# Kernel tuning notes

Measured on AMD Instinct MI355X. Metric: run time of the kernel, lower is better.

## Reference

```python
import jax, jax.numpy as jnp
import numpy as np

B, N, E, NREG, DIN, F = 16, 20000, 640000, 2000, 128, 32
NEG_SLOPE = 0.2  # PyG GATConv default negative_slope


def setup_inputs() -> dict:
    key = jax.random.key(0)
    ks = jax.random.split(key, 10)
    x = jax.random.normal(ks[0], (B, N, DIN), dtype=jnp.float32)
    edge_src = jnp.sort(jax.random.randint(ks[1], (E,), 0, NREG, dtype=jnp.int64))
    edge_dst = jax.random.randint(ks[2], (E,), 0, N, dtype=jnp.int64)
    edge_attr = jax.random.uniform(ks[3], (B, E, 1), dtype=jnp.float32)
    # GATConv parameters (heads=1, concat=False, edge_dim=1)
    W = jax.random.normal(ks[4], (DIN, F), dtype=jnp.float32) * 0.05   # lin (shared src/dst)
    att_src = jax.random.normal(ks[5], (F,), dtype=jnp.float32) * 0.1
    att_dst = jax.random.normal(ks[6], (F,), dtype=jnp.float32) * 0.1
    lin_edge = jax.random.normal(ks[7], (1, F), dtype=jnp.float32) * 0.1
    att_edge = jax.random.normal(ks[8], (F,), dtype=jnp.float32) * 0.1
    bias = jax.random.normal(ks[9], (F,), dtype=jnp.float32) * 0.01
    return {"x": x, "edge_attr": edge_attr, "W": W, "att_src": att_src,
            "att_dst": att_dst, "lin_edge": lin_edge, "att_edge": att_edge,
            "bias": bias, "edge_src": edge_src, "edge_dst": edge_dst}


def _gat_regulon(x, eattr, W, att_src, att_dst, lin_edge, att_edge, bias,
                 src, dst):
    # x: [N, DIN], eattr: [E, 1]; src/dst: [E] int (src < NREG, sorted)
    h = x @ W                                  # [N, F]
    a_src = h @ att_src                        # [N]
    a_dst = h @ att_dst                        # [N]
    # add_self_loops=True with fill_value='mean' for edge_attr
    loop_attr = jnp.broadcast_to(jnp.mean(eattr, axis=0, keepdims=True), (N, 1))
    eattr_full = jnp.concatenate([eattr, loop_attr], axis=0)         # [E+N, 1]
    sl = jnp.arange(N, dtype=src.dtype)
    src_f = jnp.concatenate([src, sl])                               # [E+N]
    dst_f = jnp.concatenate([dst, sl])                               # [E+N]
    a_edge = (eattr_full @ lin_edge) @ att_edge                      # [E+N]
    alpha = jax.nn.leaky_relu(a_src[src_f] + a_dst[dst_f] + a_edge, NEG_SLOPE)
    # segment softmax over destination nodes (self-loops => no empty segment)
    m = jax.ops.segment_max(alpha, dst_f, num_segments=N)
    ex = jnp.exp(alpha - m[dst_f])
    s = jax.ops.segment_sum(ex, dst_f, num_segments=N)
    coef = ex / s[dst_f]                                             # [E+N]
    rep = jax.ops.segment_sum(coef[:, None] * h[src_f], dst_f, num_segments=N)
    rep = rep + bias                                                 # [N, F]
    # fused regulon pooling: out[i] = rep[i] + sum_{(i->t) in E} rep[t]
    pooled = jax.ops.segment_sum(rep[dst], src, num_segments=NREG)   # [NREG, F]
    return rep[:NREG] + pooled


def reference(x, edge_attr, W, att_src, att_dst, lin_edge, att_edge, bias,
              edge_src, edge_dst):
    fn = jax.vmap(lambda xi, ei: _gat_regulon(xi, ei, W, att_src, att_dst,
                                              lin_edge, att_edge, bias,
                                              edge_src, edge_dst))
    return fn(x, edge_attr)                                          # [B, NREG, F]
```

## Files before the change

### kernel.cpp

```cpp
#include <hip/hip_runtime.h>
#include <hip/hip_fp16.h>
#include <math.h>

#define B    16
#define N    20000
#define E    640000
#define NREG 2000
#define DIN  128
#define F    32
#define NEG  0.2f
#define BF   (B * F)
#define NCHUNK 8
#define CS   2500
#define HIST_BLOCKS 1024
#define SCAT_BLOCKS 1024

typedef unsigned int uint;

__device__ inline uint f16pair(float a, float b) {
    __half2 h = __floats2half2_rn(a, b);
    return *(uint*)&h;
}
__device__ inline float2 h2f2(uint v) {
    return __half22float2(*(__half2*)&v);
}

__global__ __launch_bounds__(256) void k_prep1(const int* __restrict__ esrc,
                                               const int* __restrict__ edst,
                                               const float* __restrict__ eattr,
                                               const float* __restrict__ lin_edge,
                                               const float* __restrict__ att_edge,
                                               int* __restrict__ counts,
                                               int* __restrict__ roff,
                                               float* __restrict__ meanb,
                                               float* __restrict__ cedge) {
    int blk = blockIdx.x;
    int t = threadIdx.x;
    if (blk < HIST_BLOCKS) {
        {
            int b = blk >> 6, sl = blk & 63;
            const float4* base = (const float4*)(eattr + (size_t)b * E + sl * 10000);
            float s = 0.f;
            for (int i = t; i < 2500; i += 256) {
                float4 v = base[i];
                s += (v.x + v.y) + (v.z + v.w);
            }
            __shared__ float sh[256];
            sh[t] = s;
            __syncthreads();
            for (int d = 128; d > 0; d >>= 1) {
                if (t < d) sh[t] += sh[t + d];
                __syncthreads();
            }
            if (t == 0) atomicAdd(&meanb[b], sh[0]);
        }
        for (int e = blk * 256 + t; e < E; e += HIST_BLOCKS * 256)
            atomicAdd(&counts[edst[e]], 1);
    } else if (blk < HIST_BLOCKS + 8) {
        int r = (blk - HIST_BLOCKS) * 256 + t;
        if (r > NREG) return;
        int lo = 0, hi = E;
        while (lo < hi) {
            int mid = (lo + hi) >> 1;
            if (esrc[mid] < r) lo = mid + 1; else hi = mid;
        }
        roff[r] = lo;
    } else {
        if (t == 0) {
            float s = 0.f;
            for (int f = 0; f < F; ++f) s += lin_edge[f] * att_edge[f];
            *cedge = s;
        }
    }
}

__global__ __launch_bounds__(1024) void k_scan(const int* __restrict__ in,
                                               int* __restrict__ out, int n) {
    __shared__ int sh[1024];
    int t = threadIdx.x;
    int chunk = (n + 1023) / 1024;
    int lo = t * chunk;
    int hi = lo + chunk; if (hi > n) hi = n;
    int local = 0;
    for (int i = lo; i < hi; ++i) local += in[i];
    sh[t] = local;
    __syncthreads();
    for (int d = 1; d < 1024; d <<= 1) {
        int v = (t >= d) ? sh[t - d] : 0;
        __syncthreads();
        sh[t] += v;
        __syncthreads();
    }
    int run = (t == 0) ? 0 : sh[t - 1];
    for (int i = lo; i < hi; ++i) { out[i] = run; run += in[i]; }
    if (t == 1023) out[n] = sh[1023];
}

__global__ __launch_bounds__(256) void k_prep2(const int* __restrict__ esrc,
                                               const int* __restrict__ edst,
                                               const int* __restrict__ off,
                                               int* __restrict__ cursor,
                                               int2* __restrict__ csr_se,
                                               const int* __restrict__ roff,
                                               int* __restrict__ boff,
                                               int* __restrict__ pe_dst) {
    __shared__ int cnt[NCHUNK], pref[NCHUNK], cur[NCHUNK];
    int blk = blockIdx.x;
    int t = threadIdx.x;
    if (blk < SCAT_BLOCKS) {
        int e = blk * 256 + t;
        for (; e < E; e += SCAT_BLOCKS * 256) {
            int d = edst[e];
            int pos = off[d] + atomicAdd(&cursor[d], 1);
            csr_se[pos] = make_int2(esrc[e], e);
        }
    } else {
        int r = blk - SCAT_BLOCKS;
        int lo = roff[r], hi = roff[r + 1];
        if (t < NCHUNK) { cnt[t] = 0; cur[t] = 0; }
        __syncthreads();
        for (int e = lo + t; e < hi; e += 256)
            atomicAdd(&cnt[edst[e] / CS], 1);
        __syncthreads();
        if (t == 0) {
            int run = 0;
            #pragma unroll
            for (int c = 0; c < NCHUNK; ++c) { pref[c] = run; run += cnt[c]; }
        }
        __syncthreads();
        if (t < NCHUNK) boff[r * NCHUNK + t] = lo + pref[t];
        if (r == 0 && t == 0) boff[NREG * NCHUNK] = E;
        for (int e = lo + t; e < hi; e += 256) {
            int d = edst[e];
            int c = d / CS;
            int pos = lo + pref[c] + atomicAdd(&cur[c], 1);
            pe_dst[pos] = d;
        }
    }
}

__global__ __launch_bounds__(256) void k_trans(const float* __restrict__ eattr,
                                               const float* __restrict__ cedge,
                                               __half* __restrict__ ew) {
    __shared__ float tile[256][17];
    int e0 = blockIdx.x * 256;
    int t = threadIdx.x;
    #pragma unroll
    for (int b = 0; b < B; ++b)
        tile[t][b] = eattr[(size_t)b * E + e0 + t];
    __syncthreads();
    float c = *cedge;
    #pragma unroll
    for (int p = 0; p < 4; ++p) {
        int i4 = (p * 256 + t) * 4;
        int el = i4 >> 4, b0 = i4 & 15;
        uint2 o;
        o.x = f16pair(c * tile[el][b0 + 0], c * tile[el][b0 + 1]);
        o.y = f16pair(c * tile[el][b0 + 2], c * tile[el][b0 + 3]);
        *(uint2*)&ew[(size_t)e0 * 16 + i4] = o;
    }
}

#define XS_LD 260
__global__ __launch_bounds__(256) void k_gemm(const float* __restrict__ x,
                                              const float* __restrict__ W,
                                              const float* __restrict__ att_src,
                                              const float* __restrict__ att_dst,
                                              uint* __restrict__ hu,
                                              float* __restrict__ a_src,
                                              float* __restrict__ a_dst) {
    __shared__ float Ws[DIN * F];
    __shared__ float xs[32 * XS_LD];
    int t = threadIdx.x;
    int row0 = blockIdx.x * 256;
    #pragma unroll
    for (int j = 0; j < 4; ++j) {
        int idx = (t + 256 * j) * 4;
        *(float4*)&Ws[idx] = *(const float4*)&W[idx];
    }
    const int lr = t & 63;
    const int fg = t >> 6;
    float acc[4][8];
    #pragma unroll
    for (int i = 0; i < 4; ++i)
        #pragma unroll
        for (int j = 0; j < 8; ++j) acc[i][j] = 0.f;

    for (int kc = 0; kc < 4; ++kc) {
        __syncthreads();
        #pragma unroll
        for (int j = 0; j < 8; ++j) {
            int p = t + 256 * j;
            int row = p >> 3;
            int kk  = (p & 7) * 4;
            float4 g = *(const float4*)&x[(size_t)(row0 + row) * DIN + kc * 32 + kk];
            xs[(kk + 0) * XS_LD + row] = g.x;
            xs[(kk + 1) * XS_LD + row] = g.y;
            xs[(kk + 2) * XS_LD + row] = g.z;
            xs[(kk + 3) * XS_LD + row] = g.w;
        }
        __syncthreads();
        #pragma unroll
        for (int k = 0; k < 32; ++k) {
            float4 xv = *(float4*)&xs[k * XS_LD + 4 * lr];
            float4 w0 = *(float4*)&Ws[(kc * 32 + k) * F + fg * 8];
            float4 w1 = *(float4*)&Ws[(kc * 32 + k) * F + fg * 8 + 4];
            float xr[4] = {xv.x, xv.y, xv.z, xv.w};
            float wr[8] = {w0.x, w0.y, w0.z, w0.w, w1.x, w1.y, w1.z, w1.w};
            #pragma unroll
            for (int i = 0; i < 4; ++i)
                #pragma unroll
                for (int j = 0; j < 8; ++j)
                    acc[i][j] = fmaf(xr[i], wr[j], acc[i][j]);
        }
    }
    #pragma unroll
    for (int i = 0; i < 4; ++i) {
        int row = row0 + lr * 4 + i;
        int b = row / N;
        int n = row - b * N;
        uint4 o;
        o.x = f16pair(acc[i][0], acc[i][1]);
        o.y = f16pair(acc[i][2], acc[i][3]);
        o.z = f16pair(acc[i][4], acc[i][5]);
        o.w = f16pair(acc[i][6], acc[i][7]);
        *(uint4*)&hu[(size_t)n * 256 + b * 16 + fg * 4] = o;
    }
    float* red = xs;
    __syncthreads();
    #pragma unroll
    for (int i = 0; i < 4; ++i) {
        float s1 = 0.f, s2 = 0.f;
        #pragma unroll
        for (int j = 0; j < 8; ++j) {
            float as = att_src[fg * 8 + j];
            float ad = att_dst[fg * 8 + j];
            s1 = fmaf(acc[i][j], as, s1);
            s2 = fmaf(acc[i][j], ad, s2);
        }
        red[fg * 256 + lr * 4 + i]        = s1;
        red[1024 + fg * 256 + lr * 4 + i] = s2;
    }
    __syncthreads();
    {
        float s1 = red[t] + red[256 + t] + red[512 + t] + red[768 + t];
        float s2 = red[1024 + t] + red[1280 + t] + red[1536 + t] + red[1792 + t];
        int row = row0 + t;
        int b = row / N;
        int n = row - b * N;
        a_src[(size_t)n * B + b] = s1;
        a_dst[(size_t)n * B + b] = s2;
    }
}

__global__ __launch_bounds__(256) void k_rep(
    const uint4* __restrict__ hu4, const float* __restrict__ a_src,
    const float* __restrict__ a_dst, const __half* __restrict__ ew,
    const int2* __restrict__ csr_se, const float* __restrict__ bias,
    const float* __restrict__ meanb, const float* __restrict__ cedge,
    const int* __restrict__ dst_off, uint4* __restrict__ repu4) {
    __shared__ uint4 lacc[4][64];
    __shared__ float lsum[4][64];
    int i = blockIdx.x;
    int t = threadIdx.x;
    int wid = t >> 6;
    int l = t & 63;
    int b = l >> 2;
    int q = l & 3;
    float adst = a_dst[(size_t)i * B + b];
    int lo = dst_off[i], hi = dst_off[i + 1];
    float ssum = 0.f;
    __half2 zero2 = __half2half2(__float2half(0.f));
    __half2 acc0 = zero2, acc1 = zero2, acc2 = zero2, acc3 = zero2;

    for (int g0 = lo + wid * 4; g0 < hi; g0 += 16) {
        int jj = g0 + q;
        int idx = jj < hi ? jj : hi - 1;
        int2 se = csr_se[idx];
        float a2 = a_src[(size_t)se.x * B + b] + adst
                 + __half2float(ew[(size_t)se.y * B + b]);
        a2 = a2 > 0.f ? a2 : NEG * a2;
        float wv = (jj < hi) ? __expf(a2) : 0.f;
        ssum += wv;
        __half2 w2 = __half2half2(__float2half(wv));
        uint w2u = *(uint*)&w2;
#define REP_STEP(EIDX, CTRL) { \
        int wei = __builtin_amdgcn_mov_dpp((int)w2u, CTRL, 0xf, 0xf, true); \
        __half2 weh = *(__half2*)&wei; \
        int sre = __builtin_amdgcn_readlane(se.x, EIDX); \
        uint4 hv = hu4[(size_t)sre * 64 + l]; \
        acc0 = __hfma2(weh, *(__half2*)&hv.x, acc0); \
        acc1 = __hfma2(weh, *(__half2*)&hv.y, acc1); \
        acc2 = __hfma2(weh, *(__half2*)&hv.z, acc2); \
        acc3 = __hfma2(weh, *(__half2*)&hv.w, acc3); }
        REP_STEP(0, 0)
        REP_STEP(1, 85)
        REP_STEP(2, 170)
        REP_STEP(3, 255)
#undef REP_STEP
    }
    ssum += __shfl_xor(ssum, 1, 64);
    ssum += __shfl_xor(ssum, 2, 64);
    if (wid) {
        uint4 a;
        a.x = *(uint*)&acc0; a.y = *(uint*)&acc1;
        a.z = *(uint*)&acc2; a.w = *(uint*)&acc3;
        lacc[wid][l] = a;
        lsum[wid][l] = ssum;
    }
    __syncthreads();
    if (wid == 0) {
        float2 p0 = __half22float2(acc0);
        float2 p1 = __half22float2(acc1);
        float2 p2 = __half22float2(acc2);
        float2 p3 = __half22float2(acc3);
        #pragma unroll
        for (int ww = 1; ww < 4; ++ww) {
            uint4 a = lacc[ww][l];
            float2 u;
            u = h2f2(a.x); p0.x += u.x; p0.y += u.y;
            u = h2f2(a.y); p1.x += u.x; p1.y += u.y;
            u = h2f2(a.z); p2.x += u.x; p2.y += u.y;
            u = h2f2(a.w); p3.x += u.x; p3.y += u.y;
            ssum += lsum[ww][l];
        }
        float c = *cedge;
        float meanv = meanb[b] * (1.f / (float)E);
        float al = a_src[(size_t)i * B + b] + adst + meanv * c;
        al = al > 0.f ? al : NEG * al;
        float ws = __expf(al);
        uint4 hv = hu4[(size_t)i * 64 + l];
        float2 u;
        u = h2f2(hv.x); p0.x = fmaf(ws, u.x, p0.x); p0.y = fmaf(ws, u.y, p0.y);
        u = h2f2(hv.y); p1.x = fmaf(ws, u.x, p1.x); p1.y = fmaf(ws, u.y, p1.y);
        u = h2f2(hv.z); p2.x = fmaf(ws, u.x, p2.x); p2.y = fmaf(ws, u.y, p2.y);
        u = h2f2(hv.w); p3.x = fmaf(ws, u.x, p3.x); p3.y = fmaf(ws, u.y, p3.y);
        float inv = 1.f / (ssum + ws);
        const float4* bias4 = (const float4*)bias;
        float4 ba = bias4[q * 2];
        float4 bb = bias4[q * 2 + 1];
        uint4 o;
        o.x = f16pair(fmaf(p0.x, inv, ba.x), fmaf(p0.y, inv, ba.y));
        o.y = f16pair(fmaf(p1.x, inv, ba.z), fmaf(p1.y, inv, ba.w));
        o.z = f16pair(fmaf(p2.x, inv, bb.x), fmaf(p2.y, inv, bb.y));
        o.w = f16pair(fmaf(p3.x, inv, bb.z), fmaf(p3.y, inv, bb.w));
        repu4[(size_t)i * 64 + l] = o;
    }
}

__global__ __launch_bounds__(256) void k_pool(const uint* __restrict__ repu,
                                              const int* __restrict__ boff,
                                              const int* __restrict__ pe_dst,
                                              float* __restrict__ partial) {
    int key = blockIdx.x;
    int c = key / NREG;
    int r = key - c * NREG;
    int idx = r * NCHUNK + c;
    int t = threadIdx.x;
    int lo = boff[idx], hi = boff[idx + 1];
    float acc0 = 0.f, acc1 = 0.f;
    int e = lo;
    for (; e + 8 <= hi; e += 8) {
        int d0 = pe_dst[e+0], d1 = pe_dst[e+1], d2 = pe_dst[e+2], d3 = pe_dst[e+3];
        int d4 = pe_dst[e+4], d5 = pe_dst[e+5], d6 = pe_dst[e+6], d7 = pe_dst[e+7];
        uint v0 = repu[(size_t)d0 * 256 + t];
        uint v1 = repu[(size_t)d1 * 256 + t];
        uint v2 = repu[(size_t)d2 * 256 + t];
        uint v3 = repu[(size_t)d3 * 256 + t];
        uint v4 = repu[(size_t)d4 * 256 + t];
        uint v5 = repu[(size_t)d5 * 256 + t];
        uint v6 = repu[(size_t)d6 * 256 + t];
        uint v7 = repu[(size_t)d7 * 256 + t];
        float2 u0 = h2f2(v0), u1 = h2f2(v1), u2 = h2f2(v2), u3 = h2f2(v3);
        float2 u4 = h2f2(v4), u5 = h2f2(v5), u6 = h2f2(v6), u7 = h2f2(v7);
        acc0 += (u0.x + u1.x) + (u2.x + u3.x) + (u4.x + u5.x) + (u6.x + u7.x);
        acc1 += (u0.y + u1.y) + (u2.y + u3.y) + (u4.y + u5.y) + (u6.y + u7.y);
    }
    for (; e < hi; ++e) {
        int d = pe_dst[e];
        float2 u = h2f2(repu[(size_t)d * 256 + t]);
        acc0 += u.x;
        acc1 += u.y;
    }
    float2 o = {acc0, acc1};
    *(float2*)&partial[((size_t)r * NCHUNK + c) * BF + 2 * t] = o;
}

__global__ __launch_bounds__(256) void k_combine(const uint* __restrict__ repu,
                                                 const float* __restrict__ partial,
                                                 float* __restrict__ out) {
    int r = blockIdx.x;
    int t = threadIdx.x;
    int b  = t >> 4;
    int fp = t & 15;
    float2 u = h2f2(repu[(size_t)r * 256 + t]);
    float s0 = u.x, s1 = u.y;
    #pragma unroll
    for (int c = 0; c < NCHUNK; ++c) {
        float2 p = *(const float2*)&partial[((size_t)r * NCHUNK + c) * BF + 2 * t];
        s0 += p.x; s1 += p.y;
    }
    float2 o = {s0, s1};
    *(float2*)&out[(size_t)b * NREG * F + r * F + 2 * fp] = o;
}

extern "C" void kernel_launch(void* const* d_in, const int* in_sizes, int n_in,
                              void* d_out, int out_size, void* d_ws, size_t ws_size,
                              hipStream_t stream) {
    const float* x        = (const float*)d_in[0];
    const float* eattr    = (const float*)d_in[1];
    const float* W        = (const float*)d_in[2];
    const float* att_src  = (const float*)d_in[3];
    const float* att_dst  = (const float*)d_in[4];
    const float* lin_edge = (const float*)d_in[5];
    const float* att_edge = (const float*)d_in[6];
    const float* bias     = (const float*)d_in[7];
    const int*   esrc     = (const int*)d_in[8];
    const int*   edst     = (const int*)d_in[9];
    float* out = (float*)d_out;

    char* ws = (char*)d_ws;
    size_t off = 0;
    auto alloc = [&](size_t bytes) -> void* {
        void* p = ws + off;
        off = (off + bytes + 255) & ~(size_t)255;
        return p;
    };
    uint*  hu    = (uint*)alloc((size_t)N * 256 * 4);
    uint*  repu  = (uint*)alloc((size_t)N * 256 * 4);
    __half* ew   = (__half*)alloc((size_t)E * B * 2);
    float* partial = (float*)alloc((size_t)NREG * NCHUNK * BF * 4);
    float* a_src = (float*)alloc((size_t)N * B * 4);
    float* a_dst = (float*)alloc((size_t)N * B * 4);
    int* dst_off = (int*)alloc((size_t)(N + 1) * 4);
    int* roff    = (int*)alloc((size_t)(NREG + 1) * 4);
    int2* csr_se = (int2*)alloc((size_t)E * 8);
    int* pe_dst  = (int*)alloc((size_t)E * 4);
    int* boff    = (int*)alloc((size_t)(NREG * NCHUNK + 1) * 4);
    char* zbase   = ws + off;
    int* counts   = (int*)alloc((size_t)N * 4);
    int* cursor   = (int*)alloc((size_t)N * 4);
    float* meanb  = (float*)alloc((size_t)B * 4);
    float* cedge  = (float*)alloc(4);
    size_t zbytes = (size_t)((ws + off) - zbase);

    hipMemsetAsync(zbase, 0, zbytes, stream);

    k_prep1<<<HIST_BLOCKS + 8 + 1, 256, 0, stream>>>(esrc, edst, eattr, lin_edge,
                                                     att_edge, counts, roff,
                                                     meanb, cedge);
    k_scan<<<1, 1024, 0, stream>>>(counts, dst_off, N);
    k_prep2<<<SCAT_BLOCKS + NREG, 256, 0, stream>>>(esrc, edst, dst_off, cursor,
                                                    csr_se, roff, boff, pe_dst);
    k_gemm<<<(B * N) / 256, 256, 0, stream>>>(x, W, att_src, att_dst,
                                              hu, a_src, a_dst);
    k_trans<<<E / 256, 256, 0, stream>>>(eattr, cedge, ew);
    k_rep<<<N, 256, 0, stream>>>((const uint4*)hu, a_src, a_dst, ew, csr_se,
                                 bias, meanb, cedge, dst_off, (uint4*)repu);
    k_pool<<<NREG * NCHUNK, 256, 0, stream>>>(repu, boff, pe_dst, partial);
    k_combine<<<NREG, 256, 0, stream>>>(repu, partial, out);
}
```

Baseline: 489.0 us.

## Use fp16 MFMA for node projection GEMM and fuse with edge-weight transpose

Replaces the scalar FP32 x@W GEMM with fp16 MFMA 16x16x32 instructions. The accumulator tiles are staged through shared memory so each thread writes one full fp16 output row and computes the attention dot products itself. The edge-attribute transpose kernel is merged into the same launch as extra blocks, removing one launch and letting the two memory-bound phases overlap. Rounding x and W to fp16 before accumulation adds precision error to h and the attention logits.

New measurement: 484.5 us. Within noise of the previous version (-0.9%).

```diff
diff --git a/kernel.cpp b/kernel.cpp
--- a/kernel.cpp
+++ b/kernel.cpp
@@ -14,8 +14,11 @@
 #define CS   2500
 #define HIST_BLOCKS 1024
 #define SCAT_BLOCKS 1024
+#define GEMM_BLOCKS 1250
 
 typedef unsigned int uint;
+typedef _Float16 half8 __attribute__((ext_vector_type(8)));
+typedef float f32x4 __attribute__((ext_vector_type(4)));
 
 __device__ inline uint f16pair(float a, float b) {
     __half2 h = __floats2half2_rn(a, b);
@@ -139,117 +142,112 @@
     }
 }
 
-__global__ __launch_bounds__(256) void k_trans(const float* __restrict__ eattr,
-                                               const float* __restrict__ cedge,
-                                               __half* __restrict__ ew) {
-    __shared__ float tile[256][17];
-    int e0 = blockIdx.x * 256;
-    int t = threadIdx.x;
-    #pragma unroll
-    for (int b = 0; b < B; ++b)
-        tile[t][b] = eattr[(size_t)b * E + e0 + t];
-    __syncthreads();
-    float c = *cedge;
-    #pragma unroll
-    for (int p = 0; p < 4; ++p) {
-        int i4 = (p * 256 + t) * 4;
-        int el = i4 >> 4, b0 = i4 & 15;
-        uint2 o;
-        o.x = f16pair(c * tile[el][b0 + 0], c * tile[el][b0 + 1]);
-        o.y = f16pair(c * tile[el][b0 + 2], c * tile[el][b0 + 3]);
-        *(uint2*)&ew[(size_t)e0 * 16 + i4] = o;
-    }
-}
-
-#define XS_LD 260
-__global__ __launch_bounds__(256) void k_gemm(const float* __restrict__ x,
-                                              const float* __restrict__ W,
-                                              const float* __restrict__ att_src,
-                                              const float* __restrict__ att_dst,
-                                              uint* __restrict__ hu,
-                                              float* __restrict__ a_src,
-                                              float* __restrict__ a_dst) {
-    __shared__ float Ws[DIN * F];
-    __shared__ float xs[32 * XS_LD];
-    int t = threadIdx.x;
-    int row0 = blockIdx.x * 256;
-    #pragma unroll
-    for (int j = 0; j < 4; ++j) {
-        int idx = (t + 256 * j) * 4;
-        *(float4*)&Ws[idx] = *(const float4*)&W[idx];
-    }
-    const int lr = t & 63;
-    const int fg = t >> 6;
-    float acc[4][8];
-    #pragma unroll
-    for (int i = 0; i < 4; ++i)
-        #pragma unroll
-        for (int j = 0; j < 8; ++j) acc[i][j] = 0.f;
-
-    for (int kc = 0; kc < 4; ++kc) {
-        __syncthreads();
-        #pragma unroll
-        for (int j = 0; j < 8; ++j) {
-            int p = t + 256 * j;
-            int row = p >> 3;
-            int kk  = (p & 7) * 4;
-            float4 g = *(const float4*)&x[(size_t)(row0 + row) * DIN + kc * 32 + kk];
-            xs[(kk + 0) * XS_LD + row] = g.x;
-            xs[(kk + 1) * XS_LD + row] = g.y;
-            xs[(kk + 2) * XS_LD + row] = g.z;
-            xs[(kk + 3) * XS_LD + row] = g.w;
-        }
-        __syncthreads();
-        #pragma unroll
-        for (int k = 0; k < 32; ++k) {
-            float4 xv = *(float4*)&xs[k * XS_LD + 4 * lr];
-            float4 w0 = *(float4*)&Ws[(kc * 32 + k) * F + fg * 8];
-            float4 w1 = *(float4*)&Ws[(kc * 32 + k) * F + fg * 8 + 4];
-            float xr[4] = {xv.x, xv.y, xv.z, xv.w};
-            float wr[8] = {w0.x, w0.y, w0.z, w0.w, w1.x, w1.y, w1.z, w1.w};
-            #pragma unroll
-            for (int i = 0; i < 4; ++i)
+__global__ __launch_bounds__(256) void k_gt(const float* __restrict__ x,
+                                            const float* __restrict__ W,
+                                            const float* __restrict__ att_src,
+                                            const float* __restrict__ att_dst,
+                                            const float* __restrict__ eattr,
+                                            const float* __restrict__ cedge,
+                                            uint* __restrict__ hu,
+                                            float* __restrict__ a_src,
+                                            float* __restrict__ a_dst,
+                                            __half* __restrict__ ew) {
+    __shared__ uint smem[11392];
+    int blk = blockIdx.x;
+    int t = threadIdx.x;
+    if (blk < GEMM_BLOCKS) {
+        _Float16* Wt = (_Float16*)smem;
+        float* hbuf = (float*)(smem + 2176);
+        int wid = t >> 6;
+        int l = t & 63;
+        int row0 = blk * 256;
+        #pragma unroll
+        for (int p = 0; p < 16; ++p) {
+            int idx = p * 256 + t;
+            Wt[(idx & 31) * 136 + (idx >> 5)] = (_Float16)W[idx];
+        }
+        __syncthreads();
+        int col = l & 15, kg = l >> 4;
+        half8 bf[2][4];
+        #pragma unroll
+        for (int ct = 0; ct < 2; ++ct)
+            #pragma unroll
+            for (int kc = 0; kc < 4; ++kc)
+                bf[ct][kc] = *(half8*)&Wt[(ct * 16 + col) * 136 + kc * 32 + kg * 8];
+        f32x4 acc[4][2];
+        #pragma unroll
+        for (int rt = 0; rt < 4; ++rt)
+            #pragma unroll
+            for (int ct = 0; ct < 2; ++ct)
+                acc[rt][ct] = (f32x4){0.f, 0.f, 0.f, 0.f};
+        int rbase = row0 + wid * 64;
+        #pragma unroll
+        for (int kc = 0; kc < 4; ++kc) {
+            half8 afr[4];
+            #pragma unroll
+            for (int rt = 0; rt < 4; ++rt) {
+                const float* xp = &x[(size_t)(rbase + rt * 16 + col) * DIN + kc * 32 + kg * 8];
+                float4 xa = *(const float4*)xp;
+                float4 xb = *(const float4*)(xp + 4);
+                half8 a;
+                a[0] = (_Float16)xa.x; a[1] = (_Float16)xa.y;
+                a[2] = (_Float16)xa.z; a[3] = (_Float16)xa.w;
+                a[4] = (_Float16)xb.x; a[5] = (_Float16)xb.y;
+                a[6] = (_Float16)xb.z; a[7] = (_Float16)xb.w;
+                afr[rt] = a;
+            }
+            #pragma unroll
+            for (int rt = 0; rt < 4; ++rt)
                 #pragma unroll
-                for (int j = 0; j < 8; ++j)
-                    acc[i][j] = fmaf(xr[i], wr[j], acc[i][j]);
-        }
-    }
-    #pragma unroll
-    for (int i = 0; i < 4; ++i) {
-        int row = row0 + lr * 4 + i;
-        int b = row / N;
-        int n = row - b * N;
-        uint4 o;
-        o.x = f16pair(acc[i][0], acc[i][1]);
-        o.y = f16pair(acc[i][2], acc[i][3]);
-        o.z = f16pair(acc[i][4], acc[i][5]);
-        o.w = f16pair(acc[i][6], acc[i][7]);
-        *(uint4*)&hu[(size_t)n * 256 + b * 16 + fg * 4] = o;
-    }
-    float* red = xs;
-    __syncthreads();
-    #pragma unroll
-    for (int i = 0; i < 4; ++i) {
+                for (int ct = 0; ct < 2; ++ct)
+                    acc[rt][ct] = __builtin_amdgcn_mfma_f32_16x16x32_f16(
+                        afr[rt], bf[ct][kc], acc[rt][ct], 0, 0, 0);
+        }
+        float* hb = hbuf + wid * (64 * 36);
+        #pragma unroll
+        for (int rt = 0; rt < 4; ++rt)
+            #pragma unroll
+            for (int ct = 0; ct < 2; ++ct)
+                #pragma unroll
+                for (int m = 0; m < 4; ++m)
+                    hb[(rt * 16 + kg * 4 + m) * 36 + ct * 16 + col] = acc[rt][ct][m];
+        int row_g = rbase + l;
+        int b = row_g / N;
+        int n = row_g - b * N;
+        const float* hr = hb + l * 36;
         float s1 = 0.f, s2 = 0.f;
-        #pragma unroll
-        for (int j = 0; j < 8; ++j) {
-            float as = att_src[fg * 8 + j];
-            float ad = att_dst[fg * 8 + j];
-            s1 = fmaf(acc[i][j], as, s1);
-            s2 = fmaf(acc[i][j], ad, s2);
-        }
-        red[fg * 256 + lr * 4 + i]        = s1;
-        red[1024 + fg * 256 + lr * 4 + i] = s2;
-    }
-    __syncthreads();
-    {
-        float s1 = red[t] + red[256 + t] + red[512 + t] + red[768 + t];
-        float s2 = red[1024 + t] + red[1280 + t] + red[1536 + t] + red[1792 + t];
-        int row = row0 + t;
-        int b = row / N;
-        int n = row - b * N;
+        uint ou[16];
+        #pragma unroll
+        for (int j = 0; j < 16; ++j) {
+            float e0 = hr[2 * j], e1 = hr[2 * j + 1];
+            ou[j] = f16pair(e0, e1);
+            s1 = fmaf(e0, att_src[2 * j], fmaf(e1, att_src[2 * j + 1], s1));
+            s2 = fmaf(e0, att_dst[2 * j], fmaf(e1, att_dst[2 * j + 1], s2));
+        }
+        uint4* dst = (uint4*)&hu[(size_t)n * 256 + b * 16];
+        dst[0] = make_uint4(ou[0], ou[1], ou[2], ou[3]);
+        dst[1] = make_uint4(ou[4], ou[5], ou[6], ou[7]);
+        dst[2] = make_uint4(ou[8], ou[9], ou[10], ou[11]);
+        dst[3] = make_uint4(ou[12], ou[13], ou[14], ou[15]);
         a_src[(size_t)n * B + b] = s1;
         a_dst[(size_t)n * B + b] = s2;
+    } else {
+        float (*tile)[17] = (float(*)[17])smem;
+        int e0 = (blk - GEMM_BLOCKS) * 256;
+        #pragma unroll
+        for (int b = 0; b < B; ++b)
+            tile[t][b] = eattr[(size_t)b * E + e0 + t];
+        __syncthreads();
+        float c = *cedge;
+        #pragma unroll
+        for (int p = 0; p < 4; ++p) {
+            int i4 = (p * 256 + t) * 4;
+            int el = i4 >> 4, b0 = i4 & 15;
+            uint2 o;
+            o.x = f16pair(c * tile[el][b0 + 0], c * tile[el][b0 + 1]);
+            o.y = f16pair(c * tile[el][b0 + 2], c * tile[el][b0 + 3]);
+            *(uint2*)&ew[(size_t)e0 * 16 + i4] = o;
+        }
     }
 }
 
@@ -452,9 +450,9 @@
     k_scan<<<1, 1024, 0, stream>>>(counts, dst_off, N);
     k_prep2<<<SCAT_BLOCKS + NREG, 256, 0, stream>>>(esrc, edst, dst_off, cursor,
                                                     csr_se, roff, boff, pe_dst);
-    k_gemm<<<(B * N) / 256, 256, 0, stream>>>(x, W, att_src, att_dst,
-                                              hu, a_src, a_dst);
-    k_trans<<<E / 256, 256, 0, stream>>>(eattr, cedge, ew);
+    k_gt<<<GEMM_BLOCKS + E / 256, 256, 0, stream>>>(x, W, att_src, att_dst,
+                                                    eattr, cedge, hu,
+                                                    a_src, a_dst, ew);
     k_rep<<<N, 256, 0, stream>>>((const uint4*)hu, a_src, a_dst, ew, csr_se,
                                  bias, meanb, cedge, dst_off, (uint4*)repu);
     k_pool<<<NREG * NCHUNK, 256, 0, stream>>>(repu, boff, pe_dst, partial);
```
